# Performance work log

Hardware: AMD Instinct MI355X
Metric: run time of the kernel (lower is better)

Reference implementation:

```python
import jax, jax.numpy as jnp
import numpy as np

N = 50000      # nodes
E = 1600000    # edges (before self loops)
IN = 128       # in_channels
HID = 64       # hidden_channels
OUT = 16       # out_channels
NEG_SLOPE = 0.2


def gat_conv(x, edge_index, W, a_src, a_dst, bias, heads, ch):
    """PyG GATConv: linear -> per-edge attention (LeakyReLU) -> segment softmax
    over destination nodes -> scatter-add aggregation. add_self_loops=True."""
    n = x.shape[0]
    loop = jnp.arange(n, dtype=edge_index.dtype)
    src = jnp.concatenate([edge_index[0], loop])  # [Etot]
    dst = jnp.concatenate([edge_index[1], loop])
    h = (x @ W).reshape(n, heads, ch)             # [N,H,C]
    asrc = jnp.sum(h * a_src, axis=-1)            # [N,H]
    adst = jnp.sum(h * a_dst, axis=-1)            # [N,H]
    e = jax.nn.leaky_relu(asrc[src] + adst[dst], NEG_SLOPE)      # [Etot,H]
    emax = jax.ops.segment_max(e, dst, num_segments=n)           # [N,H]
    emax = jnp.where(jnp.isfinite(emax), emax, 0.0)
    p = jnp.exp(e - emax[dst])
    denom = jax.ops.segment_sum(p, dst, num_segments=n)          # [N,H]
    alpha = p / (denom[dst] + 1e-16)                             # [Etot,H]
    out = jax.ops.segment_sum(h[src] * alpha[:, :, None], dst, num_segments=n)
    return out.reshape(n, heads * ch) + bias      # concat (heads=1 is a no-op)


def setup_inputs() -> dict:
    key = jax.random.key(0)
    ks = jax.random.split(key, 12)
    s = 0.05
    return {
        "x": jax.random.normal(ks[0], (N, IN), dtype=jnp.float32),
        "edge_index": jax.random.randint(ks[1], (2, E), 0, N, dtype=jnp.int64),
        # conv1: heads=2
        "W1": jax.random.normal(ks[2], (IN, 2 * HID), dtype=jnp.float32) * s,
        "a_src1": jax.random.normal(ks[3], (2, HID), dtype=jnp.float32) * s,
        "a_dst1": jax.random.normal(ks[4], (2, HID), dtype=jnp.float32) * s,
        "b1": jnp.zeros((2 * HID,), dtype=jnp.float32),
        # conv2: heads=1, in = 2*HID
        "W2": jax.random.normal(ks[5], (2 * HID, HID), dtype=jnp.float32) * s,
        "a_src2": jax.random.normal(ks[6], (1, HID), dtype=jnp.float32) * s,
        "a_dst2": jax.random.normal(ks[7], (1, HID), dtype=jnp.float32) * s,
        "b2": jnp.zeros((HID,), dtype=jnp.float32),
        # final linear
        "Wl": jax.random.normal(ks[8], (HID, OUT), dtype=jnp.float32) * s,
        "bl": jnp.zeros((OUT,), dtype=jnp.float32),
    }


def reference(x, edge_index, W1, a_src1, a_dst1, b1, W2, a_src2, a_dst2, b2, Wl, bl):
    h = jax.nn.relu(gat_conv(x, edge_index, W1, a_src1, a_dst1, b1, heads=2, ch=HID))
    # dropout p=0.3: identity at inference (deterministic reference)
    h = jax.nn.relu(gat_conv(h, edge_index, W2, a_src2, a_dst2, b2, heads=1, ch=HID))
    return h @ Wl + bl
```

## Files before the change

### kernel.cpp

```cpp
#include <hip/hip_runtime.h>
#include <hip/hip_fp16.h>

#define NEG 0.2f
#define RW 512
#define RSH 9
#define RCAP 18432


template <int K, int M, int H, bool PART>
__global__ __launch_bounds__(256) void k_gemm(const float* __restrict__ X,
                                              const float* __restrict__ W,
                                              const float* __restrict__ a_src,
                                              const float* __restrict__ a_dst,
                                              __half* __restrict__ Yh,
                                              float* __restrict__ asrc,
                                              float* __restrict__ adst, int n,
                                              const int* __restrict__ esrc,
                                              const int* __restrict__ edst, int E, int NRg,
                                              int* rcur, unsigned int* part) {
    constexpr int KH = 64;
    __shared__ float Ws[KH * M];
    __shared__ float Xs[32][K + 4];
    __shared__ int ph[128];
    __shared__ int pb[128];
    int tid = threadIdx.x;
    int row0 = blockIdx.x * 32;

    if (PART && blockIdx.x * 2048 < E) {
        int i0 = (blockIdx.x * 256 + tid) * 8;
        int ds[8], ss[8];
        if (i0 + 7 < E) {
            int4 a = *reinterpret_cast<const int4*>(&edst[i0]);
            int4 b = *reinterpret_cast<const int4*>(&edst[i0 + 4]);
            ds[0] = a.x; ds[1] = a.y; ds[2] = a.z; ds[3] = a.w;
            ds[4] = b.x; ds[5] = b.y; ds[6] = b.z; ds[7] = b.w;
            int4 c = *reinterpret_cast<const int4*>(&esrc[i0]);
            int4 d = *reinterpret_cast<const int4*>(&esrc[i0 + 4]);
            ss[0] = c.x; ss[1] = c.y; ss[2] = c.z; ss[3] = c.w;
            ss[4] = d.x; ss[5] = d.y; ss[6] = d.z; ss[7] = d.w;
        } else {
#pragma unroll
            for (int j = 0; j < 8; j++) {
                ds[j] = (i0 + j < E) ? edst[i0 + j] : 0;
                ss[j] = (i0 + j < E) ? esrc[i0 + j] : 0;
            }
        }
        if (tid < NRg) ph[tid] = 0;
        __syncthreads();
#pragma unroll
        for (int j = 0; j < 8; j++)
            if (i0 + j < E) atomicAdd(&ph[ds[j] >> RSH], 1);
        __syncthreads();
        if (tid < NRg) {
            int c = ph[tid];
            pb[tid] = c ? atomicAdd(&rcur[tid], c) : 0;
            ph[tid] = 0;
        }
        __syncthreads();
#pragma unroll
        for (int j = 0; j < 8; j++) {
            if (i0 + j < E) {
                int r = ds[j] >> RSH;
                int rk = atomicAdd(&ph[r], 1) + pb[r];
                if (rk < RCAP)
                    part[(size_t)r * RCAP + rk] =
                        ((unsigned int)(ds[j] & (RW - 1)) << 16) | (unsigned int)(ss[j] & 0xFFFF);
            }
        }
    }

    for (int idx = tid; idx < 32 * (K / 4); idx += 256) {
        int r = idx / (K / 4), c4 = idx % (K / 4);
        int gr = row0 + r;
        float4 v = make_float4(0.f, 0.f, 0.f, 0.f);
        if (gr < n) v = *reinterpret_cast<const float4*>(&X[(size_t)gr * K + c4 * 4]);
        *reinterpret_cast<float4*>(&Xs[r][c4 * 4]) = v;
    }

    constexpr int NJ = M / 32;
    float4 acc[NJ];
#pragma unroll
    for (int j = 0; j < NJ; j++) acc[j] = make_float4(0.f, 0.f, 0.f, 0.f);
    int r = tid >> 3, cg = tid & 7;

    for (int kh = 0; kh < K; kh += KH) {
        __syncthreads();
        for (int idx = tid; idx < (KH * M) / 4; idx += 256) {
            *reinterpret_cast<float4*>(&Ws[idx * 4]) =
                *reinterpret_cast<const float4*>(&W[(size_t)kh * M + idx * 4]);
        }
        __syncthreads();
        for (int k = 0; k < KH; k++) {
            float xv = Xs[r][kh + k];
#pragma unroll
            for (int j = 0; j < NJ; j++) {
                float4 wv = *reinterpret_cast<const float4*>(&Ws[k * M + cg * 4 + j * 32]);
                acc[j].x += xv * wv.x;
                acc[j].y += xv * wv.y;
                acc[j].z += xv * wv.z;
                acc[j].w += xv * wv.w;
            }
        }
    }

    int gr = row0 + r;
    if (gr < n) {
#pragma unroll
        for (int j = 0; j < NJ; j++) {
            union {
                __half2 h2[2];
                uint2 u;
            } cv;
            cv.h2[0] = __floats2half2_rn(acc[j].x, acc[j].y);
            cv.h2[1] = __floats2half2_rn(acc[j].z, acc[j].w);
            *reinterpret_cast<uint2*>(&Yh[(size_t)gr * M + cg * 4 + j * 32]) = cv.u;
        }
    }

    float ps0 = 0.f, pd0 = 0.f, ps1 = 0.f, pd1 = 0.f;
#pragma unroll
    for (int j = 0; j < NJ; j++) {
        int colb = cg * 4 + j * 32;
        float4 av = *reinterpret_cast<const float4*>(&a_src[colb]);
        float4 dv = *reinterpret_cast<const float4*>(&a_dst[colb]);
        float s = acc[j].x * av.x + acc[j].y * av.y + acc[j].z * av.z + acc[j].w * av.w;
        float d = acc[j].x * dv.x + acc[j].y * dv.y + acc[j].z * dv.z + acc[j].w * dv.w;
        if (H == 2 && j >= NJ / 2) {
            ps1 += s;
            pd1 += d;
        } else {
            ps0 += s;
            pd0 += d;
        }
    }
#pragma unroll
    for (int m = 1; m < 8; m <<= 1) {
        ps0 += __shfl_xor(ps0, m, 64);
        pd0 += __shfl_xor(pd0, m, 64);
        if (H == 2) {
            ps1 += __shfl_xor(ps1, m, 64);
            pd1 += __shfl_xor(pd1, m, 64);
        }
    }
    if (gr < n && cg == 0) {
        if (H == 2) {
            *reinterpret_cast<float2*>(&asrc[gr * 2]) = make_float2(ps0, ps1);
            *reinterpret_cast<float2*>(&adst[gr * 2]) = make_float2(pd0, pd1);
        } else {
            asrc[gr] = ps0;
            adst[gr] = pd0;
        }
    }
}


__global__ __launch_bounds__(512) void k_build(const unsigned int* __restrict__ part,
                                               const int* __restrict__ rcur, int n,
                                               unsigned short* __restrict__ csr,
                                               int* __restrict__ rowptr) {
    __shared__ int hist[RW];
    __shared__ int wsum[8];
    __shared__ int rbase_s;
    int r = blockIdx.x;
    int tid = threadIdx.x, lane = tid & 63, wid = tid >> 6;
    int cnt = min(rcur[r], RCAP);
    if (tid == 0) {
        int b = 0;
        for (int j = 0; j < r; j++) b += min(rcur[j], RCAP);
        rbase_s = b;
    }
    hist[tid] = 0;
    __syncthreads();
    int rbase = rbase_s;
    const unsigned int* pr = part + (size_t)r * RCAP;

    for (int i = tid; i < cnt; i += 512) atomicAdd(&hist[pr[i] >> 16], 1);
    __syncthreads();

    int v = hist[tid];
    int incl = v;
#pragma unroll
    for (int m = 1; m < 64; m <<= 1) {
        int t = __shfl_up(incl, m, 64);
        if (lane >= m) incl += t;
    }
    if (lane == 63) wsum[wid] = incl;
    __syncthreads();
    if (wid == 0) {
        int s = (lane < 8) ? wsum[lane] : 0;
#pragma unroll
        for (int m = 1; m < 8; m <<= 1) {
            int t = __shfl_up(s, m, 64);
            if (lane >= m) s += t;
        }
        if (lane < 8) wsum[lane] = s;
    }
    __syncthreads();
    int excl = (incl - v) + (wid > 0 ? wsum[wid - 1] : 0);
    __syncthreads();
    hist[tid] = excl;
    int g = r * RW + tid;
    if (g < n) rowptr[g] = rbase + excl;
    if (r == gridDim.x - 1 && tid == 0) rowptr[n] = rbase + cnt;
    __syncthreads();

    for (int i = tid; i < cnt; i += 512) {
        unsigned int e = pr[i];
        int rk = atomicAdd(&hist[e >> 16], 1);
        csr[rbase + rk] = (unsigned short)(e & 0xFFFF);
    }
}


__global__ __launch_bounds__(256) void k_gat2(const __half* __restrict__ hh,
                                              const float* __restrict__ asrc,
                                              const float* __restrict__ adst,
                                              const int* __restrict__ rowptr,
                                              const unsigned short* __restrict__ csr_src,
                                              const float* __restrict__ bias,
                                              float* __restrict__ out, int n) {
    int node = blockIdx.x * 4 + (threadIdx.x >> 6);
    int lane = threadIdx.x & 63;
    if (node >= n) return;

    int beg = rowptr[node], end = rowptr[node + 1];
    float2 adn = *reinterpret_cast<const float2*>(&adst[node * 2]);
    float2 asn = *reinterpret_cast<const float2*>(&asrc[node * 2]);
    float e0 = asn.x + adn.x;
    e0 = e0 > 0.f ? e0 : NEG * e0;
    float e1 = asn.y + adn.y;
    e1 = e1 > 0.f ? e1 : NEG * e1;
    float pself0 = __expf(e0), pself1 = __expf(e1);

    int g = lane >> 4;
    int lc = lane & 15;
    bool head1 = lc >= 8;

    float4 sraw = *reinterpret_cast<const float4*>(&hh[(size_t)node * 128 + lc * 8]);

    float2 acc[4];
#pragma unroll
    for (int k = 0; k < 4; k++) acc[k] = make_float2(0.f, 0.f);
    float psum0 = 0.f, psum1 = 0.f;

    for (int base = beg; base < end; base += 64) {
        int i = base + lane;
        int cnt = min(64, end - base);
        float p0 = 0.f, p1 = 0.f;
        int s = 0;
        if (i < end) {
            s = (int)csr_src[i];
            float2 a2 = *reinterpret_cast<const float2*>(&asrc[s * 2]);
            float f0 = a2.x + adn.x;
            f0 = f0 > 0.f ? f0 : NEG * f0;
            float f1 = a2.y + adn.y;
            f1 = f1 > 0.f ? f1 : NEG * f1;
            p0 = __expf(f0);
            p1 = __expf(f1);
            psum0 += p0;
            psum1 += p1;
        }
        int nt = (cnt + 3) >> 2;
#pragma unroll 8
        for (int t = 0; t < nt; t++) {
            int ej = t * 4 + g;
            int sj = __shfl(s, ej, 64);
            float pj0 = __shfl(p0, ej, 64);
            float pj1 = __shfl(p1, ej, 64);
            float pj = head1 ? pj1 : pj0;
            if (ej < cnt) {
                float4 raw = *reinterpret_cast<const float4*>(&hh[(size_t)sj * 128 + lc * 8]);
                const __half2* hp = reinterpret_cast<const __half2*>(&raw);
#pragma unroll
                for (int k = 0; k < 4; k++) {
                    float2 f = __half22float2(hp[k]);
                    acc[k].x += pj * f.x;
                    acc[k].y += pj * f.y;
                }
            }
        }
    }

#pragma unroll
    for (int m = 1; m < 64; m <<= 1) {
        psum0 += __shfl_xor(psum0, m, 64);
        psum1 += __shfl_xor(psum1, m, 64);
    }
    float inv0 = 1.f / (psum0 + pself0 + 1e-16f);
    float inv1 = 1.f / (psum1 + pself1 + 1e-16f);

#pragma unroll
    for (int m = 16; m < 64; m <<= 1) {
#pragma unroll
        for (int k = 0; k < 4; k++) {
            acc[k].x += __shfl_xor(acc[k].x, m, 64);
            acc[k].y += __shfl_xor(acc[k].y, m, 64);
        }
    }

    float inv = head1 ? inv1 : inv0;
    float pself = head1 ? pself1 : pself0;
    const __half2* sp = reinterpret_cast<const __half2*>(&sraw);
    float4 b0 = *reinterpret_cast<const float4*>(&bias[lc * 8]);
    float4 b1 = *reinterpret_cast<const float4*>(&bias[lc * 8 + 4]);
    float o[8];
#pragma unroll
    for (int k = 0; k < 4; k++) {
        float2 f = __half22float2(sp[k]);
        o[2 * k] = (acc[k].x + pself * f.x) * inv;
        o[2 * k + 1] = (acc[k].y + pself * f.y) * inv;
    }
    o[0] = fmaxf(o[0] + b0.x, 0.f);
    o[1] = fmaxf(o[1] + b0.y, 0.f);
    o[2] = fmaxf(o[2] + b0.z, 0.f);
    o[3] = fmaxf(o[3] + b0.w, 0.f);
    o[4] = fmaxf(o[4] + b1.x, 0.f);
    o[5] = fmaxf(o[5] + b1.y, 0.f);
    o[6] = fmaxf(o[6] + b1.z, 0.f);
    o[7] = fmaxf(o[7] + b1.w, 0.f);

    if (lane < 16) {
        float* op = &out[(size_t)node * 128 + lc * 8];
        *reinterpret_cast<float4*>(op) = make_float4(o[0], o[1], o[2], o[3]);
        *reinterpret_cast<float4*>(op + 4) = make_float4(o[4], o[5], o[6], o[7]);
    }
}


__global__ __launch_bounds__(256) void k_gat1(const __half* __restrict__ hh,
                                              const float* __restrict__ asrc,
                                              const float* __restrict__ adst,
                                              const int* __restrict__ rowptr,
                                              const unsigned short* __restrict__ csr_src,
                                              const float* __restrict__ bias,
                                              const float* __restrict__ Wl,
                                              const float* __restrict__ bl,
                                              float* __restrict__ out, int n) {
    __shared__ float Wls[64 * 16];
    __shared__ float bls[16];
    __shared__ float hbuf[4][64];
    int tid = threadIdx.x;
    for (int i = tid; i < 64 * 16; i += 256) Wls[i] = Wl[i];
    if (tid < 16) bls[tid] = bl[tid];
    __syncthreads();

    int w = tid >> 6, lane = tid & 63;
    int node = blockIdx.x * 4 + w;
    if (node >= n) return;

    int beg = rowptr[node], end = rowptr[node + 1];
    float adn = adst[node];
    float e0 = asrc[node] + adn;
    e0 = e0 > 0.f ? e0 : NEG * e0;
    float pself = __expf(e0);

    int g = lane >> 3;
    int lc = lane & 7;

    float4 sraw = *reinterpret_cast<const float4*>(&hh[(size_t)node * 64 + lc * 8]);

    float2 acc[4];
#pragma unroll
    for (int k = 0; k < 4; k++) acc[k] = make_float2(0.f, 0.f);
    float psum = 0.f;

    for (int base = beg; base < end; base += 64) {
        int i = base + lane;
        int cnt = min(64, end - base);
        float p = 0.f;
        int s = 0;
        if (i < end) {
            s = (int)csr_src[i];
            float e = asrc[s] + adn;
            e = e > 0.f ? e : NEG * e;
            p = __expf(e);
            psum += p;
        }
        int nt = (cnt + 7) >> 3;
#pragma unroll 8
        for (int t = 0; t < nt; t++) {
            int ej = t * 8 + g;
            int sj = __shfl(s, ej, 64);
            float pj = __shfl(p, ej, 64);
            if (ej < cnt) {
                float4 raw = *reinterpret_cast<const float4*>(&hh[(size_t)sj * 64 + lc * 8]);
                const __half2* hp = reinterpret_cast<const __half2*>(&raw);
#pragma unroll
                for (int k = 0; k < 4; k++) {
                    float2 f = __half22float2(hp[k]);
                    acc[k].x += pj * f.x;
                    acc[k].y += pj * f.y;
                }
            }
        }
    }

#pragma unroll
    for (int m = 1; m < 64; m <<= 1) psum += __shfl_xor(psum, m, 64);
    float inv = 1.f / (psum + pself + 1e-16f);

#pragma unroll
    for (int m = 8; m < 64; m <<= 1) {
#pragma unroll
        for (int k = 0; k < 4; k++) {
            acc[k].x += __shfl_xor(acc[k].x, m, 64);
            acc[k].y += __shfl_xor(acc[k].y, m, 64);
        }
    }

    const __half2* sp = reinterpret_cast<const __half2*>(&sraw);
    float4 b0 = *reinterpret_cast<const float4*>(&bias[lc * 8]);
    float4 b1 = *reinterpret_cast<const float4*>(&bias[lc * 8 + 4]);
    float o[8];
#pragma unroll
    for (int k = 0; k < 4; k++) {
        float2 f = __half22float2(sp[k]);
        o[2 * k] = (acc[k].x + pself * f.x) * inv;
        o[2 * k + 1] = (acc[k].y + pself * f.y) * inv;
    }
    o[0] = fmaxf(o[0] + b0.x, 0.f);
    o[1] = fmaxf(o[1] + b0.y, 0.f);
    o[2] = fmaxf(o[2] + b0.z, 0.f);
    o[3] = fmaxf(o[3] + b0.w, 0.f);
    o[4] = fmaxf(o[4] + b1.x, 0.f);
    o[5] = fmaxf(o[5] + b1.y, 0.f);
    o[6] = fmaxf(o[6] + b1.z, 0.f);
    o[7] = fmaxf(o[7] + b1.w, 0.f);

    if (lane < 8) {
        float* hp = &hbuf[w][lc * 8];
        *reinterpret_cast<float4*>(hp) = make_float4(o[0], o[1], o[2], o[3]);
        *reinterpret_cast<float4*>(hp + 4) = make_float4(o[4], o[5], o[6], o[7]);
    }
    __builtin_amdgcn_wave_barrier();

    int col = lane & 15, q = lane >> 4;
    float a = 0.f;
#pragma unroll
    for (int k = 0; k < 16; k++) {
        int kk = q * 16 + k;
        a += hbuf[w][kk] * Wls[kk * 16 + col];
    }
    a += __shfl_xor(a, 16, 64);
    a += __shfl_xor(a, 32, 64);
    if (lane < 16) out[(size_t)node * 16 + col] = a + bls[col];
}


extern "C" void kernel_launch(void* const* d_in, const int* in_sizes, int n_in,
                              void* d_out, int out_size, void* d_ws, size_t ws_size,
                              hipStream_t stream) {
    const float* x      = (const float*)d_in[0];
    const int*   ei     = (const int*)d_in[1];
    const float* W1     = (const float*)d_in[2];
    const float* a_src1 = (const float*)d_in[3];
    const float* a_dst1 = (const float*)d_in[4];
    const float* b1     = (const float*)d_in[5];
    const float* W2     = (const float*)d_in[6];
    const float* a_src2 = (const float*)d_in[7];
    const float* a_dst2 = (const float*)d_in[8];
    const float* b2     = (const float*)d_in[9];
    const float* Wl     = (const float*)d_in[10];
    const float* bl     = (const float*)d_in[11];
    float* out = (float*)d_out;

    int n = in_sizes[0] / 128;
    int E = in_sizes[1] / 2;
    const int* src = ei;
    const int* dst = ei + E;
    int NRg = (n + RW - 1) >> RSH;

    char* w = (char*)d_ws;
    size_t off = 0;
    auto alloc = [&](size_t bytes) {
        void* p = w + off;
        off = (off + bytes + 255) & ~(size_t)255;
        return p;
    };
    int*            rcur   = (int*)alloc(128 * 4);
    unsigned int*   part   = (unsigned int*)alloc((size_t)NRg * RCAP * 4);
    int*            rowptr = (int*)alloc((size_t)(n + 1) * 4);
    unsigned short* csr    = (unsigned short*)alloc((size_t)E * 2);
    __half*         h1h    = (__half*)alloc((size_t)n * 128 * 2);
    float*          as1    = (float*)alloc((size_t)n * 2 * 4);
    float*          ad1    = (float*)alloc((size_t)n * 2 * 4);
    float*          hm     = (float*)alloc((size_t)n * 128 * 4);
    __half*         h2h    = (__half*)alloc((size_t)n * 64 * 2);
    float*          as2    = (float*)alloc((size_t)n * 4);
    float*          ad2    = (float*)alloc((size_t)n * 4);

    hipMemsetAsync(rcur, 0, 128 * 4, stream);

    int gblocks = (n + 31) / 32;
    int bblocks = (E + 2047) / 2048;
    int grid1 = gblocks > bblocks ? gblocks : bblocks;

    k_gemm<128, 128, 2, true><<<grid1, 256, 0, stream>>>(x, W1, a_src1, a_dst1, h1h, as1, ad1, n,
                                                         src, dst, E, NRg, rcur, part);
    k_build<<<NRg, 512, 0, stream>>>(part, rcur, n, csr, rowptr);
    k_gat2<<<(n + 3) / 4, 256, 0, stream>>>(h1h, as1, ad1, rowptr, csr, b1, hm, n);

    k_gemm<128, 64, 1, false><<<gblocks, 256, 0, stream>>>(hm, W2, a_src2, a_dst2, h2h, as2, ad2, n,
                                                           nullptr, nullptr, 0, 0, nullptr, nullptr);
    k_gat1<<<(n + 3) / 4, 256, 0, stream>>>(h2h, as2, ad2, rowptr, csr, b2, Wl, bl, out, n);
}
```

Measured before the change: 222.8 us.

## Remap GEMM threads to contiguous columns with multi-row register tiles

Rewrites the thread mapping in the fused GEMM+attention-logit kernel. Each thread now owns one 4-column quad and several rows, loading X as float4 along K so each W vector is reused across rows. KH drops to 32, which shrinks the W shared tile and raises occupancy. The attention dot-product reduction now shuffles across 16 lanes per head. The partition scratch arrays move into the PART branch scope. This trades more register accumulators per thread for fewer shared-memory loads per FMA.

```diff
diff --git a/kernel.cpp b/kernel.cpp
--- a/kernel.cpp
+++ b/kernel.cpp
@@ -18,15 +18,18 @@
                                               const int* __restrict__ esrc,
                                               const int* __restrict__ edst, int E, int NRg,
                                               int* rcur, unsigned int* part) {
-    constexpr int KH = 64;
+    constexpr int KH = 32;
+    constexpr int NCQ = M / 4;
+    constexpr int NRG = 256 / NCQ;
+    constexpr int RPT = 32 / NRG;
     __shared__ float Ws[KH * M];
     __shared__ float Xs[32][K + 4];
-    __shared__ int ph[128];
-    __shared__ int pb[128];
     int tid = threadIdx.x;
     int row0 = blockIdx.x * 32;
 
     if (PART && blockIdx.x * 2048 < E) {
+        __shared__ int ph[128];
+        __shared__ int pb[128];
         int i0 = (blockIdx.x * 256 + tid) * 8;
         int ds[8], ss[8];
         if (i0 + 7 < E) {
@@ -77,11 +80,10 @@
         *reinterpret_cast<float4*>(&Xs[r][c4 * 4]) = v;
     }
 
-    constexpr int NJ = M / 32;
-    float4 acc[NJ];
-#pragma unroll
-    for (int j = 0; j < NJ; j++) acc[j] = make_float4(0.f, 0.f, 0.f, 0.f);
-    int r = tid >> 3, cg = tid & 7;
+    int rg = tid / NCQ, cq = tid % NCQ;
+    float4 acc[RPT];
+#pragma unroll
+    for (int r2 = 0; r2 < RPT; r2++) acc[r2] = make_float4(0.f, 0.f, 0.f, 0.f);
 
     for (int kh = 0; kh < K; kh += KH) {
         __syncthreads();
@@ -90,65 +92,78 @@
                 *reinterpret_cast<const float4*>(&W[(size_t)kh * M + idx * 4]);
         }
         __syncthreads();
-        for (int k = 0; k < KH; k++) {
-            float xv = Xs[r][kh + k];
-#pragma unroll
-            for (int j = 0; j < NJ; j++) {
-                float4 wv = *reinterpret_cast<const float4*>(&Ws[k * M + cg * 4 + j * 32]);
-                acc[j].x += xv * wv.x;
-                acc[j].y += xv * wv.y;
-                acc[j].z += xv * wv.z;
-                acc[j].w += xv * wv.w;
-            }
-        }
-    }
-
-    int gr = row0 + r;
-    if (gr < n) {
-#pragma unroll
-        for (int j = 0; j < NJ; j++) {
+        for (int k4 = 0; k4 < KH; k4 += 4) {
+            float4 xq[RPT];
+#pragma unroll
+            for (int r2 = 0; r2 < RPT; r2++)
+                xq[r2] = *reinterpret_cast<const float4*>(&Xs[rg * RPT + r2][kh + k4]);
+#pragma unroll
+            for (int kk = 0; kk < 4; kk++) {
+                float4 wv = *reinterpret_cast<const float4*>(&Ws[(k4 + kk) * M + cq * 4]);
+#pragma unroll
+                for (int r2 = 0; r2 < RPT; r2++) {
+                    float xs = kk == 0 ? xq[r2].x : kk == 1 ? xq[r2].y : kk == 2 ? xq[r2].z : xq[r2].w;
+                    acc[r2].x += xs * wv.x;
+                    acc[r2].y += xs * wv.y;
+                    acc[r2].z += xs * wv.z;
+                    acc[r2].w += xs * wv.w;
+                }
+            }
+        }
+    }
+
+#pragma unroll
+    for (int r2 = 0; r2 < RPT; r2++) {
+        int gr = row0 + rg * RPT + r2;
+        if (gr < n) {
             union {
                 __half2 h2[2];
                 uint2 u;
             } cv;
-            cv.h2[0] = __floats2half2_rn(acc[j].x, acc[j].y);
-            cv.h2[1] = __floats2half2_rn(acc[j].z, acc[j].w);
-            *reinterpret_cast<uint2*>(&Yh[(size_t)gr * M + cg * 4 + j * 32]) = cv.u;
-        }
-    }
-
-    float ps0 = 0.f, pd0 = 0.f, ps1 = 0.f, pd1 = 0.f;
-#pragma unroll
-    for (int j = 0; j < NJ; j++) {
-        int colb = cg * 4 + j * 32;
-        float4 av = *reinterpret_cast<const float4*>(&a_src[colb]);
-        float4 dv = *reinterpret_cast<const float4*>(&a_dst[colb]);
-        float s = acc[j].x * av.x + acc[j].y * av.y + acc[j].z * av.z + acc[j].w * av.w;
-        float d = acc[j].x * dv.x + acc[j].y * dv.y + acc[j].z * dv.z + acc[j].w * dv.w;
-        if (H == 2 && j >= NJ / 2) {
-            ps1 += s;
-            pd1 += d;
-        } else {
-            ps0 += s;
-            pd0 += d;
-        }
-    }
-#pragma unroll
-    for (int m = 1; m < 8; m <<= 1) {
-        ps0 += __shfl_xor(ps0, m, 64);
-        pd0 += __shfl_xor(pd0, m, 64);
-        if (H == 2) {
-            ps1 += __shfl_xor(ps1, m, 64);
-            pd1 += __shfl_xor(pd1, m, 64);
-        }
-    }
-    if (gr < n && cg == 0) {
-        if (H == 2) {
-            *reinterpret_cast<float2*>(&asrc[gr * 2]) = make_float2(ps0, ps1);
-            *reinterpret_cast<float2*>(&adst[gr * 2]) = make_float2(pd0, pd1);
-        } else {
-            asrc[gr] = ps0;
-            adst[gr] = pd0;
+            cv.h2[0] = __floats2half2_rn(acc[r2].x, acc[r2].y);
+            cv.h2[1] = __floats2half2_rn(acc[r2].z, acc[r2].w);
+            *reinterpret_cast<uint2*>(&Yh[(size_t)gr * M + cq * 4]) = cv.u;
+        }
+    }
+
+    float4 av = *reinterpret_cast<const float4*>(&a_src[cq * 4]);
+    float4 dv = *reinterpret_cast<const float4*>(&a_dst[cq * 4]);
+    float ps[RPT], pd[RPT];
+#pragma unroll
+    for (int r2 = 0; r2 < RPT; r2++) {
+        ps[r2] = acc[r2].x * av.x + acc[r2].y * av.y + acc[r2].z * av.z + acc[r2].w * av.w;
+        pd[r2] = acc[r2].x * dv.x + acc[r2].y * dv.y + acc[r2].z * dv.z + acc[r2].w * dv.w;
+    }
+#pragma unroll
+    for (int m = 1; m < 16; m <<= 1) {
+#pragma unroll
+        for (int r2 = 0; r2 < RPT; r2++) {
+            ps[r2] += __shfl_xor(ps[r2], m, 64);
+            pd[r2] += __shfl_xor(pd[r2], m, 64);
+        }
+    }
+    if (H == 2) {
+        if ((cq & 15) == 0) {
+            int head = cq >> 4;
+#pragma unroll
+            for (int r2 = 0; r2 < RPT; r2++) {
+                int gr = row0 + rg * RPT + r2;
+                if (gr < n) {
+                    asrc[gr * 2 + head] = ps[r2];
+                    adst[gr * 2 + head] = pd[r2];
+                }
+            }
+        }
+    } else {
+        if (cq == 0) {
+#pragma unroll
+            for (int r2 = 0; r2 < RPT; r2++) {
+                int gr = row0 + rg * RPT + r2;
+                if (gr < n) {
+                    asrc[gr] = ps[r2];
+                    adst[gr] = pd[r2];
+                }
+            }
         }
     }
 }
```

Result: slower. 369.9 us (+66.1%).
